# Kernel optimization log

Measured on AMD Instinct MI355X. Metric: run time of the kernel, lower is better.

## Reference

```python
import jax, jax.numpy as jnp
import numpy as np

B, D, H = 4096, 256, 1024
TRACE_STEPS = 10
T_FINAL = 1.0


def setup_inputs() -> dict:
    key = jax.random.key(0)
    k0, k1, k2 = jax.random.split(key, 3)
    s1 = 1.0 / np.sqrt(D + 1)
    s2 = 1.0 / np.sqrt(H)
    return {
        "x": jax.random.normal(k0, (B, D), dtype=jnp.float32),
        "W1": jax.random.uniform(k1, (D + 1, H), jnp.float32, -s1, s1),
        "b1": jnp.zeros((H,), jnp.float32),
        "W2": jax.random.uniform(k2, (H, D), jnp.float32, -s2, s2),
        "b2": jnp.zeros((D,), jnp.float32),
    }


def _odefun(params, t, z):
    # FFJORD vector field: tanh MLP on [z, t]. z: [B, D] -> [B, D]
    W1, b1, W2, b2 = params
    tcol = jnp.full((z.shape[0], 1), t, dtype=z.dtype)
    h = jnp.tanh(jnp.concatenate([z, tcol], axis=-1) @ W1 + b1)
    return h @ W2 + b2


def _rademacher(key, shape, dtype):
    # randint(0,2)*2-1, matching the torch probe construction
    return jax.random.randint(key, shape, 0, 2).astype(dtype) * 2.0 - 1.0


def _aug_dynamics(params, t, state, e):
    # state: [B, D+1] = [z | logp]; e: [TRACE_STEPS, B, D] Rademacher probes.
    # torch computes etf = grad((f*e).sum(), z) = e^T J, div = (e^T J)*e summed.
    # e^T J e == e . (J e), so forward-mode jvp gives identical math.
    z = state[:, :-1]
    f = lambda zz: _odefun(params, t, zz)

    def probe(ei):
        f_z, Je = jax.jvp(f, (z,), (ei,))
        return f_z, jnp.sum(Je * ei, axis=-1)  # [B]

    f_z, divs = jax.vmap(probe)(e)
    f_z = f_z[0]                       # primal identical across probes
    div_est = jnp.mean(divs, axis=0)   # average of trace_steps estimates
    return jnp.concatenate([f_z, -div_est[:, None]], axis=-1)


def reference(x, W1, b1, W2, b2):
    params = (W1, b1, W2, b2)
    Bx = x.shape[0]
    ekey = jax.random.key(42)
    probes = lambda i: _rademacher(jax.random.fold_in(ekey, i), (TRACE_STEPS, Bx, D), x.dtype)

    # initial augmented state: [z, logp=0]
    y0 = jnp.concatenate([x, jnp.zeros((Bx, 1), x.dtype)], axis=-1)

    # t_grid = [0, T] with 2 points -> fixed-grid rk4 takes ONE RK4 step of size T
    h = T_FINAL
    g = lambda t, y, i: _aug_dynamics(params, t, y, probes(i))
    k1 = g(0.0, y0, 0)
    k2 = g(0.5 * h, y0 + 0.5 * h * k1, 1)
    k3 = g(0.5 * h, y0 + 0.5 * h * k2, 2)
    k4 = g(h, y0 + h * k3, 3)
    y1 = y0 + (h / 6.0) * (k1 + 2.0 * k2 + 2.0 * k3 + k4)

    # module returns the full trajectory `output`: [len(t_grid), B, D+1]
    return jnp.stack([y0, y1], axis=0)
```

## Files before the change

kernel.cpp:

```cpp
#include <hip/hip_runtime.h>
#include <stdint.h>

#define BATCH 4096
#define DIMD  256
#define DIMH  1024
#define NEEL  10485760
#define NSLOT 1310720

typedef __attribute__((ext_vector_type(8))) short short8;
typedef __attribute__((ext_vector_type(4))) float float4v;

struct Keys4 { uint32_t a[4]; uint32_t b[4]; };

__host__ __device__ static inline uint32_t rotl32(uint32_t v, int r) {
#ifdef __HIP_DEVICE_COMPILE__
    return __builtin_amdgcn_alignbit(v, v, 32 - r);
#else
    return (v << r) | (v >> (32 - r));
#endif
}

__host__ __device__ static inline void tf2x32(uint32_t k0, uint32_t k1,
                                              uint32_t c0, uint32_t c1,
                                              uint32_t& o0, uint32_t& o1) {
    uint32_t ks0 = k0, ks1 = k1, ks2 = k0 ^ k1 ^ 0x1BD11BDAu;
    uint32_t x0 = c0 + ks0, x1 = c1 + ks1;
#define TF_R4(a, b, c, d)                                   \
    x0 += x1; x1 = rotl32(x1, a); x1 ^= x0;                 \
    x0 += x1; x1 = rotl32(x1, b); x1 ^= x0;                 \
    x0 += x1; x1 = rotl32(x1, c); x1 ^= x0;                 \
    x0 += x1; x1 = rotl32(x1, d); x1 ^= x0;
    TF_R4(13, 15, 26, 6)  x0 += ks1; x1 += ks2 + 1u;
    TF_R4(17, 29, 16, 24) x0 += ks2; x1 += ks0 + 2u;
    TF_R4(13, 15, 26, 6)  x0 += ks0; x1 += ks1 + 3u;
    TF_R4(17, 29, 16, 24) x0 += ks1; x1 += ks2 + 4u;
    TF_R4(13, 15, 26, 6)  x0 += ks2; x1 += ks0 + 5u;
#undef TF_R4
    o0 = x0; o1 = x1;
}

__device__ static inline short f2bf(float f) {
    uint32_t u = __float_as_uint(f);
    uint32_t r = (u + 0x7FFFu + ((u >> 16) & 1u)) >> 16;
    return (short)r;
}

__device__ static inline void egen_slot(short* __restrict__ EF, uint32_t q,
                                        uint32_t k0, uint32_t k1) {
    const uint32_t lane = q & 63u;
    const uint32_t ks   = (q >> 6) & 7u;
    const uint32_t T    = (q >> 9) & 255u;
    const uint32_t probe = q >> 17;
    const uint32_t b = T * 16u + (lane & 15u);
    const uint32_t d0 = ks * 32u + (lane >> 4) * 8u;
    const uint32_t jbase = (probe * 4096u + b) * 256u + d0;
    short8 val;
#pragma unroll
    for (int jj = 0; jj < 8; ++jj) {
        uint32_t y0, y1;
        tf2x32(k0, k1, 0u, jbase + (uint32_t)jj, y0, y1);
        val[jj] = ((y0 ^ y1) & 1u) ? (short)0x3F80 : (short)0xBF80u;
    }
    *(short8*)&EF[(size_t)q * 8] = val;
}

__global__ __launch_bounds__(256) void k_prep(
    const float* __restrict__ x,  const float* __restrict__ W1,
    const float* __restrict__ W2, short* __restrict__ W1T,
    short* __restrict__ W2B, short* __restrict__ W2T,
    short* __restrict__ zb, float* __restrict__ dv,
    short* __restrict__ E0, uint32_t ek0, uint32_t ek1)
{
    const int idx = blockIdx.x * 256 + threadIdx.x;
    if (idx < 262144) {
        const int n = idx >> 8, d = idx & 255;
        W1T[idx] = f2bf(W1[d * DIMH + n]);
    } else if (idx < 524288) {
        const int i = idx - 262144;
        W2B[i] = f2bf(W2[i]);
    } else if (idx < 786432) {
        const int i = idx - 524288;
        const int d = i >> 10, k = i & 1023;
        W2T[i] = f2bf(W2[k * DIMD + d]);
    } else if (idx < 1835008) {
        const int i = idx - 786432;
        zb[i] = f2bf(x[i]);
    } else if (idx < 1851392) {
        dv[idx - 1835008] = 0.0f;
    } else {
        egen_slot(E0, (uint32_t)(idx - 1851392), ek0, ek1);
    }
}

__global__ __launch_bounds__(512, 4) void k_pre_div(
    const short* __restrict__ Zb, const short* __restrict__ W1T,
    const short* __restrict__ W2B, const float* __restrict__ W1,
    const float* __restrict__ b1, float tval,
    const short* __restrict__ Ecur, short* __restrict__ h_bf,
    float* __restrict__ divacc,
    short* __restrict__ Enext, uint32_t nk0, uint32_t nk1, int do_egen)
{
    __shared__ short8 Es[4096];
    const int t = threadIdx.x;
    const int b0 = blockIdx.x * 64;
    const int ntp = blockIdx.y;
    const int wave = t >> 6, lane = t & 63;
    const int col = lane & 15, kq = lane >> 4;
    const int n = ntp * 128 + wave * 16 + col;

    short8 bufr[8], bvfr[8];
#pragma unroll
    for (int ks = 0; ks < 8; ++ks) {
        bufr[ks] = *(const short8*)&W1T[n * DIMD + ks * 32 + kq * 8];
        bvfr[ks] = *(const short8*)&W2B[n * DIMD + ks * 32 + kq * 8];
    }

    float sreg[4][4];
    const float add = tval * W1[DIMD * DIMH + n] + b1[n];
#pragma unroll
    for (int ms = 0; ms < 4; ++ms) {
        float4v acc = {0.f, 0.f, 0.f, 0.f};
#pragma unroll
        for (int ks = 0; ks < 8; ++ks) {
            short8 af = *(const short8*)&Zb[(b0 + ms * 16 + col) * DIMD + ks * 32 + kq * 8];
            acc = __builtin_amdgcn_mfma_f32_16x16x32_bf16(af, bufr[ks], acc, 0, 0, 0);
        }
#pragma unroll
        for (int r = 0; r < 4; ++r) {
            float hv = tanhf(acc[r] + add);
            h_bf[(b0 + ms * 16 + kq * 4 + r) * DIMH + n] = f2bf(hv);
            sreg[ms][r] = 1.0f - hv * hv;
        }
    }

    float rowacc[4][4];
#pragma unroll
    for (int a = 0; a < 4; ++a)
#pragma unroll
        for (int r = 0; r < 4; ++r) rowacc[a][r] = 0.0f;

    const uint32_t bflat = (uint32_t)(blockIdx.y * 64 + blockIdx.x);
    const uint32_t qbase = bflat * 512u + (uint32_t)t;

    const int Tb = b0 >> 4;

#pragma unroll 1
    for (int pp = 0; pp < 5; ++pp) {
        if (do_egen) {
            egen_slot(Enext, qbase + (uint32_t)pp * 262144u, nk0, nk1);
        }
        const short8* src0 = (const short8*)Ecur + (size_t)((2 * pp) * 256 + Tb) * 512;
        const short8* src1 = src0 + (size_t)256 * 512;
        __syncthreads();
#pragma unroll
        for (int k = 0; k < 4; ++k)
            Es[t + k * 512] = src0[t + k * 512];
#pragma unroll
        for (int k = 0; k < 4; ++k)
            Es[2048 + t + k * 512] = src1[t + k * 512];
        __syncthreads();

#pragma unroll
        for (int half = 0; half < 2; ++half) {
#pragma unroll
            for (int ms = 0; ms < 4; ++ms) {
                float4v u = {0.f, 0.f, 0.f, 0.f}, v = {0.f, 0.f, 0.f, 0.f};
#pragma unroll
                for (int ks = 0; ks < 8; ++ks) {
                    short8 af = Es[half * 2048 + ((ms * 8 + ks) << 6) + lane];
                    u = __builtin_amdgcn_mfma_f32_16x16x32_bf16(af, bufr[ks], u, 0, 0, 0);
                    v = __builtin_amdgcn_mfma_f32_16x16x32_bf16(af, bvfr[ks], v, 0, 0, 0);
                }
#pragma unroll
                for (int r = 0; r < 4; ++r)
                    rowacc[ms][r] += u[r] * sreg[ms][r] * v[r];
            }
        }
    }

#pragma unroll
    for (int ms = 0; ms < 4; ++ms) {
#pragma unroll
        for (int r = 0; r < 4; ++r) {
            float p = rowacc[ms][r];
            p += __shfl_xor(p, 1, 64);
            p += __shfl_xor(p, 2, 64);
            p += __shfl_xor(p, 4, 64);
            p += __shfl_xor(p, 8, 64);
            rowacc[ms][r] = p;
        }
    }
    if (col == 0) {
#pragma unroll
        for (int ms = 0; ms < 4; ++ms)
#pragma unroll
            for (int r = 0; r < 4; ++r)
                atomicAdd(&divacc[b0 + ms * 16 + kq * 4 + r], rowacc[ms][r] * 0.1f);
    }
}

__global__ __launch_bounds__(256) void k_fz2(
    const short* __restrict__ Hb, const short* __restrict__ W2T,
    const float* __restrict__ b2, const float* __restrict__ x,
    float* __restrict__ rksum, float cw, int first,
    float cnext, int write_zb, short* __restrict__ zb,
    int final_out, const float* __restrict__ dv, float* __restrict__ out)
{
    const int t = threadIdx.x;
    const int wave = t >> 6, lane = t & 63;
    const int col = lane & 15, kq = lane >> 4;
    const int m0 = blockIdx.x * 16;
    const int n0 = blockIdx.y * 64 + wave * 16;
    const int TOT = BATCH * (DIMD + 1);
    const float sixth = 1.0f / 6.0f;

    float4v acc = {0.f, 0.f, 0.f, 0.f};

    const short* ap = &Hb[(m0 + col) * DIMH + kq * 8];
    const short* bp = &W2T[(n0 + col) * DIMH + kq * 8];
    short8 a_cur = *(const short8*)ap;
    short8 b_cur = *(const short8*)bp;

    for (int ks = 0; ks < 31; ++ks) {
        short8 a_nxt = *(const short8*)&ap[(ks + 1) * 32];
        short8 b_nxt = *(const short8*)&bp[(ks + 1) * 32];
        acc = __builtin_amdgcn_mfma_f32_16x16x32_bf16(a_cur, b_cur, acc, 0, 0, 0);
        a_cur = a_nxt;
        b_cur = b_nxt;
    }
    acc = __builtin_amdgcn_mfma_f32_16x16x32_bf16(a_cur, b_cur, acc, 0, 0, 0);

    {
        const int nn = n0 + col;
        const float bias = b2[nn];
#pragma unroll
        for (int r = 0; r < 4; ++r) {
            const int m = m0 + kq * 4 + r;
            const int o = m * DIMD + nn;
            const float val = acc[r] + bias;
            if (final_out) {
                const float xv = x[o];
                out[m * (DIMD + 1) + nn] = xv;
                out[TOT + m * (DIMD + 1) + nn] =
                    xv + (rksum[o] + val) * sixth;
            } else {
                const float contrib = cw * val;
                rksum[o] = first ? contrib : (rksum[o] + contrib);
                if (write_zb)
                    zb[o] = f2bf(x[o] + cnext * val);
            }
        }
    }

    if (final_out && blockIdx.y == 0 && wave == 0 && col == 0) {
#pragma unroll
        for (int r = 0; r < 4; ++r) {
            const int m = m0 + kq * 4 + r;
            const float d1 = dv[m];
            const float d2 = dv[BATCH + m];
            const float d3 = dv[2 * BATCH + m];
            const float d4 = dv[3 * BATCH + m];
            out[m * (DIMD + 1) + DIMD] = 0.0f;
            out[TOT + m * (DIMD + 1) + DIMD] =
                -(d1 + 2.0f * d2 + 2.0f * d3 + d4) * sixth;
        }
    }
}

extern "C" void kernel_launch(void* const* d_in, const int* in_sizes, int n_in,
                              void* d_out, int out_size, void* d_ws, size_t ws_size,
                              hipStream_t stream) {
    const float* x  = (const float*)d_in[0];
    const float* W1 = (const float*)d_in[1];
    const float* b1 = (const float*)d_in[2];
    const float* W2 = (const float*)d_in[3];
    const float* b2 = (const float*)d_in[4];
    float* out = (float*)d_out;

    char* ws = (char*)d_ws;
    short* hb    = (short*)(ws);
    float* rksum = (float*)(ws + 8388608);
    short* zb    = (short*)(ws + 12582912);
    short* w1t   = (short*)(ws + 14680064);
    short* w2b   = (short*)(ws + 15204352);
    short* w2t   = (short*)(ws + 15728640);
    float* dv    = (float*)(ws + 16252928);
    short* e0    = (short*)(ws + 16318464);
    short* e1    = (short*)(ws + 37289984);

    Keys4 keys;
    for (uint32_t i = 0; i < 4; ++i) {
        uint32_t f0, f1, g0, g1;
        tf2x32(0u, 42u, 0u, i, f0, f1);
        tf2x32(f0, f1, 0u, 1u, g0, g1);
        keys.a[i] = g0;
        keys.b[i] = g1;
    }

    k_prep<<<12352, 256, 0, stream>>>(x, W1, W2, w1t, w2b, w2t, zb, dv,
                                      e0, keys.a[0], keys.b[0]);

    const float tvals[4] = {0.0f, 0.5f, 0.5f, 1.0f};
    const float cnext[4] = {0.5f, 0.5f, 1.0f, 0.0f};
    const float cw[4]    = {1.0f, 2.0f, 2.0f, 1.0f};
    for (int s = 0; s < 4; ++s) {
        const int last = (s == 3);
        short* ecur = (s & 1) ? e1 : e0;
        short* enxt = (s & 1) ? e0 : e1;
        k_pre_div<<<dim3(64, 8), 512, 0, stream>>>(
            zb, w1t, w2b, W1, b1, tvals[s], ecur,
            hb, dv + (size_t)s * BATCH,
            enxt, last ? 0u : keys.a[s + 1], last ? 0u : keys.b[s + 1],
            last ? 0 : 1);
        k_fz2<<<dim3(256, 4), 256, 0, stream>>>(hb, w2t, b2, x, rksum,
                                                cw[s], (s == 0) ? 1 : 0,
                                                cnext[s], (s < 3) ? 1 : 0, zb,
                                                last ? 1 : 0, dv, out);
    }
}
```

Measured before the change: 534.8 us.

## Halve k_pre_div waves, giving each wave two hidden-column tiles

k_pre_div now runs 4 waves per block instead of 8. Each wave holds W1/W2 fragments for two 16-column hidden tiles (n and n+64), so every probe fragment loaded from LDS feeds four MFMAs instead of two. The intent is to raise LDS reuse and MFMA density per wave and halve per-block wave count. The cost is doubled register use (fragment and accumulator arrays) and lower occupancy, with launch bounds changed to (256,2) and the cooperative LDS load and egen indexing remapped to match.

```diff
diff --git a/kernel.cpp b/kernel.cpp
--- a/kernel.cpp
+++ b/kernel.cpp
@@ -92,7 +92,7 @@
     }
 }
 
-__global__ __launch_bounds__(512, 4) void k_pre_div(
+__global__ __launch_bounds__(256, 2) void k_pre_div(
     const short* __restrict__ Zb, const short* __restrict__ W1T,
     const short* __restrict__ W2B, const float* __restrict__ W1,
     const float* __restrict__ b1, float tval,
@@ -106,74 +106,91 @@
     const int ntp = blockIdx.y;
     const int wave = t >> 6, lane = t & 63;
     const int col = lane & 15, kq = lane >> 4;
-    const int n = ntp * 128 + wave * 16 + col;
-
-    short8 bufr[8], bvfr[8];
+    const int nA = ntp * 128 + wave * 16 + col;
+    const int nB = nA + 64;
+
+    short8 bufr[2][8], bvfr[2][8];
 #pragma unroll
     for (int ks = 0; ks < 8; ++ks) {
-        bufr[ks] = *(const short8*)&W1T[n * DIMD + ks * 32 + kq * 8];
-        bvfr[ks] = *(const short8*)&W2B[n * DIMD + ks * 32 + kq * 8];
-    }
-
-    float sreg[4][4];
-    const float add = tval * W1[DIMD * DIMH + n] + b1[n];
+        bufr[0][ks] = *(const short8*)&W1T[nA * DIMD + ks * 32 + kq * 8];
+        bvfr[0][ks] = *(const short8*)&W2B[nA * DIMD + ks * 32 + kq * 8];
+        bufr[1][ks] = *(const short8*)&W1T[nB * DIMD + ks * 32 + kq * 8];
+        bvfr[1][ks] = *(const short8*)&W2B[nB * DIMD + ks * 32 + kq * 8];
+    }
+
+    float sreg[2][4][4];
+    const float addA = tval * W1[DIMD * DIMH + nA] + b1[nA];
+    const float addB = tval * W1[DIMD * DIMH + nB] + b1[nB];
 #pragma unroll
     for (int ms = 0; ms < 4; ++ms) {
-        float4v acc = {0.f, 0.f, 0.f, 0.f};
+        float4v accA = {0.f, 0.f, 0.f, 0.f}, accB = {0.f, 0.f, 0.f, 0.f};
 #pragma unroll
         for (int ks = 0; ks < 8; ++ks) {
             short8 af = *(const short8*)&Zb[(b0 + ms * 16 + col) * DIMD + ks * 32 + kq * 8];
-            acc = __builtin_amdgcn_mfma_f32_16x16x32_bf16(af, bufr[ks], acc, 0, 0, 0);
+            accA = __builtin_amdgcn_mfma_f32_16x16x32_bf16(af, bufr[0][ks], accA, 0, 0, 0);
+            accB = __builtin_amdgcn_mfma_f32_16x16x32_bf16(af, bufr[1][ks], accB, 0, 0, 0);
         }
 #pragma unroll
         for (int r = 0; r < 4; ++r) {
-            float hv = tanhf(acc[r] + add);
-            h_bf[(b0 + ms * 16 + kq * 4 + r) * DIMH + n] = f2bf(hv);
-            sreg[ms][r] = 1.0f - hv * hv;
-        }
-    }
-
-    float rowacc[4][4];
-#pragma unroll
-    for (int a = 0; a < 4; ++a)
-#pragma unroll
-        for (int r = 0; r < 4; ++r) rowacc[a][r] = 0.0f;
+            const int row = b0 + ms * 16 + kq * 4 + r;
+            float hvA = tanhf(accA[r] + addA);
+            float hvB = tanhf(accB[r] + addB);
+            h_bf[row * DIMH + nA] = f2bf(hvA);
+            h_bf[row * DIMH + nB] = f2bf(hvB);
+            sreg[0][ms][r] = 1.0f - hvA * hvA;
+            sreg[1][ms][r] = 1.0f - hvB * hvB;
+        }
+    }
+
+    float rowacc[2][4][4];
+#pragma unroll
+    for (int tt = 0; tt < 2; ++tt)
+#pragma unroll
+        for (int a = 0; a < 4; ++a)
+#pragma unroll
+            for (int r = 0; r < 4; ++r) rowacc[tt][a][r] = 0.0f;
 
     const uint32_t bflat = (uint32_t)(blockIdx.y * 64 + blockIdx.x);
-    const uint32_t qbase = bflat * 512u + (uint32_t)t;
+    const uint32_t qt = bflat * 256u + (uint32_t)t;
 
     const int Tb = b0 >> 4;
 
 #pragma unroll 1
     for (int pp = 0; pp < 5; ++pp) {
         if (do_egen) {
-            egen_slot(Enext, qbase + (uint32_t)pp * 262144u, nk0, nk1);
+            egen_slot(Enext, (uint32_t)(2 * pp) * 131072u + qt, nk0, nk1);
+            egen_slot(Enext, (uint32_t)(2 * pp + 1) * 131072u + qt, nk0, nk1);
         }
         const short8* src0 = (const short8*)Ecur + (size_t)((2 * pp) * 256 + Tb) * 512;
         const short8* src1 = src0 + (size_t)256 * 512;
         __syncthreads();
 #pragma unroll
-        for (int k = 0; k < 4; ++k)
-            Es[t + k * 512] = src0[t + k * 512];
-#pragma unroll
-        for (int k = 0; k < 4; ++k)
-            Es[2048 + t + k * 512] = src1[t + k * 512];
+        for (int k = 0; k < 8; ++k)
+            Es[t + k * 256] = src0[t + k * 256];
+#pragma unroll
+        for (int k = 0; k < 8; ++k)
+            Es[2048 + t + k * 256] = src1[t + k * 256];
         __syncthreads();
 
 #pragma unroll
         for (int half = 0; half < 2; ++half) {
 #pragma unroll
             for (int ms = 0; ms < 4; ++ms) {
-                float4v u = {0.f, 0.f, 0.f, 0.f}, v = {0.f, 0.f, 0.f, 0.f};
+                float4v uA = {0.f, 0.f, 0.f, 0.f}, vA = {0.f, 0.f, 0.f, 0.f};
+                float4v uB = {0.f, 0.f, 0.f, 0.f}, vB = {0.f, 0.f, 0.f, 0.f};
 #pragma unroll
                 for (int ks = 0; ks < 8; ++ks) {
                     short8 af = Es[half * 2048 + ((ms * 8 + ks) << 6) + lane];
-                    u = __builtin_amdgcn_mfma_f32_16x16x32_bf16(af, bufr[ks], u, 0, 0, 0);
-                    v = __builtin_amdgcn_mfma_f32_16x16x32_bf16(af, bvfr[ks], v, 0, 0, 0);
+                    uA = __builtin_amdgcn_mfma_f32_16x16x32_bf16(af, bufr[0][ks], uA, 0, 0, 0);
+                    vA = __builtin_amdgcn_mfma_f32_16x16x32_bf16(af, bvfr[0][ks], vA, 0, 0, 0);
+                    uB = __builtin_amdgcn_mfma_f32_16x16x32_bf16(af, bufr[1][ks], uB, 0, 0, 0);
+                    vB = __builtin_amdgcn_mfma_f32_16x16x32_bf16(af, bvfr[1][ks], vB, 0, 0, 0);
                 }
 #pragma unroll
-                for (int r = 0; r < 4; ++r)
-                    rowacc[ms][r] += u[r] * sreg[ms][r] * v[r];
+                for (int r = 0; r < 4; ++r) {
+                    rowacc[0][ms][r] += uA[r] * sreg[0][ms][r] * vA[r];
+                    rowacc[1][ms][r] += uB[r] * sreg[1][ms][r] * vB[r];
+                }
             }
         }
     }
@@ -182,12 +199,12 @@
     for (int ms = 0; ms < 4; ++ms) {
 #pragma unroll
         for (int r = 0; r < 4; ++r) {
-            float p = rowacc[ms][r];
+            float p = rowacc[0][ms][r] + rowacc[1][ms][r];
             p += __shfl_xor(p, 1, 64);
             p += __shfl_xor(p, 2, 64);
             p += __shfl_xor(p, 4, 64);
             p += __shfl_xor(p, 8, 64);
-            rowacc[ms][r] = p;
+            rowacc[0][ms][r] = p;
         }
     }
     if (col == 0) {
@@ -195,7 +212,7 @@
         for (int ms = 0; ms < 4; ++ms)
 #pragma unroll
             for (int r = 0; r < 4; ++r)
-                atomicAdd(&divacc[b0 + ms * 16 + kq * 4 + r], rowacc[ms][r] * 0.1f);
+                atomicAdd(&divacc[b0 + ms * 16 + kq * 4 + r], rowacc[0][ms][r] * 0.1f);
     }
 }
 
@@ -307,7 +324,7 @@
         const int last = (s == 3);
         short* ecur = (s & 1) ? e1 : e0;
         short* enxt = (s & 1) ? e0 : e1;
-        k_pre_div<<<dim3(64, 8), 512, 0, stream>>>(
+        k_pre_div<<<dim3(64, 8), 256, 0, stream>>>(
             zb, w1t, w2b, W1, b1, tvals[s], ecur,
             hb, dv + (size_t)s * BATCH,
             enxt, last ? 0u : keys.a[s + 1], last ? 0u : keys.b[s + 1],
```

After: 532.5 us. No clear change (-0.4%).
